# Kernel tuning notes

Hardware: AMD Instinct MI355X
Metric: run time of the kernel (lower is better)

The kernel has to match this reference:

```python
import jax, jax.numpy as jnp
import numpy as np

N = 1024          # n_nodes
F = 32            # n_input_features (per-node embedding dim)
HID = 64          # n_hidden_features
OUT = 32          # n_output_features


def setup_inputs() -> dict:
    key = jax.random.key(0)
    k = jax.random.split(key, 7)
    Edges = jax.random.uniform(k[0], (N, N), dtype=jnp.float32)
    Coordinates = jax.random.normal(k[1], (N, 3), dtype=jnp.float32)
    Embeddings = jax.random.normal(k[2], (N, F), dtype=jnp.float32)
    # nn.Linear params: W (out, in), b (out,)
    s1 = 1.0 / np.sqrt(2 * F)
    s2 = 1.0 / np.sqrt(HID)
    W1 = jax.random.uniform(k[3], (HID, 2 * F), dtype=jnp.float32, minval=-s1, maxval=s1)
    b1 = jax.random.uniform(k[4], (HID,), dtype=jnp.float32, minval=-s1, maxval=s1)
    W2 = jax.random.uniform(k[5], (OUT, HID), dtype=jnp.float32, minval=-s2, maxval=s2)
    b2 = jax.random.uniform(k[6], (OUT,), dtype=jnp.float32, minval=-s2, maxval=s2)
    return {"Edges": Edges, "Coordinates": Coordinates, "Embeddings": Embeddings,
            "W1": W1, "b1": b1, "W2": W2, "b2": b2}


def _swish(x):
    return x * jax.nn.sigmoid(x)


def reference(Edges, Coordinates, Embeddings, W1, b1, W2, b2):
    # pairwise euclidean distances (torch.cdist p=2), grad-safe on the zero diagonal
    diff = Coordinates[:, None, :] - Coordinates[None, :, :]          # (N, N, 3)
    sq = jnp.sum(diff * diff, axis=-1)                                # (N, N)
    dist = jnp.where(sq > 0, jnp.sqrt(jnp.where(sq > 0, sq, 1.0)), 0.0)
    w = Edges * dist                                                  # (N, N)

    # H[i, j] = concat(Emb[i], Emb[j]); first Linear applied without
    # materializing the (N, N, 2F) tensor:
    # (w * [h_i, h_j]) @ W1^T = w * (h_i @ W1[:, :F]^T + h_j @ W1[:, F:]^T)
    A = Embeddings @ W1[:, :F].T                                      # (N, HID) from h_i half
    B = Embeddings @ W1[:, F:].T                                      # (N, HID) from h_j half
    pre1 = w[:, :, None] * (A[:, None, :] + B[None, :, :]) + b1       # (N, N, HID)
    h1 = _swish(pre1)
    pre2 = jnp.einsum('ijh,oh->ijo', h1, W2) + b2                     # (N, N, OUT)
    return _swish(pre2)                                               # squeeze() is a no-op (OUT > 1)
```

## Files before the change

kernel.cpp:

```cpp
#include <hip/hip_runtime.h>
#include <math.h>

#define NN   1024
#define FF   32
#define HID  64
#define OUTF 32

typedef unsigned int  uint;
typedef unsigned short ushort;
typedef __attribute__((ext_vector_type(8)))  __bf16 bf16x8;
typedef __attribute__((ext_vector_type(16))) float  floatx16;

#define WS_A    0
#define WS_B    (WS_A + NN*HID)
#define WS_C4   (WS_B + NN*HID)
#define WS_B1   (WS_C4 + NN*4)
#define WS_B2   (WS_B1 + HID)
#define WS_W2H  (WS_B2 + 64)
#define WS_W2L  (WS_W2H + 1024)

union FragU { ushort u[8]; bf16x8 v; };

__device__ __forceinline__ float swish(float x) {
    float e = __builtin_amdgcn_exp2f(x * -1.442695040888963f);
    return x * __builtin_amdgcn_rcpf(1.0f + e);
}

__global__ void prep_kernel(
    const float* __restrict__ Coords,
    const float* __restrict__ Emb,
    const float* __restrict__ W1,
    const float* __restrict__ b1,
    const float* __restrict__ W2,
    const float* __restrict__ b2,
    float* __restrict__ ws)
{
    const int b = blockIdx.x;
    const int t = threadIdx.x;
    if (b < NN) {
        float accA = 0.f, accB = 0.f;
        const float* w1row = W1 + t * (2 * FF);
        const float* erow  = Emb + b * FF;
        #pragma unroll
        for (int f = 0; f < FF; ++f) {
            float e = erow[f];
            accA = fmaf(e, w1row[f],      accA);
            accB = fmaf(e, w1row[FF + f], accB);
        }
        ws[WS_A + b * HID + t] = accA;
        ws[WS_B + b * HID + t] = accB;
    } else {
        if (t < HID)  ws[WS_B1 + t] = b1[t];
        if (t < OUTF) ws[WS_B2 + t] = b2[t];
        #pragma unroll 1
        for (int n = t; n < NN; n += 64) {
            ws[WS_C4 + n * 4 + 0] = Coords[n * 3 + 0];
            ws[WS_C4 + n * 4 + 1] = Coords[n * 3 + 1];
            ws[WS_C4 + n * 4 + 2] = Coords[n * 3 + 2];
            ws[WS_C4 + n * 4 + 3] = 0.f;
        }
        ushort* w2h = (ushort*)(ws + WS_W2H);
        ushort* w2l = (ushort*)(ws + WS_W2L);
        const int n  = t & 31;
        const int kh = (t >> 5) * 8;
        #pragma unroll
        for (int c = 0; c < 4; ++c) {
            #pragma unroll
            for (int j = 0; j < 8; ++j) {
                const int k = c * 16 + kh + j;
                const float v = W2[n * HID + k];
                const uint  x = __float_as_uint(v);
                const float lo = v - __uint_as_float(x & 0xffff0000u);
                w2h[(c * 64 + t) * 8 + j] = (ushort)(x >> 16);
                w2l[(c * 64 + t) * 8 + j] = (ushort)(__float_as_uint(lo) >> 16);
            }
        }
    }
}

__global__ __launch_bounds__(256) void main_kernel(
    const float* __restrict__ Edges,
    const float* __restrict__ ws,
    float* __restrict__ out)
{
    const int lane = threadIdx.x & 63;
    const int wave = threadIdx.x >> 6;
    const int i    = blockIdx.y;
    const int j0   = blockIdx.x * 128 + wave * 32;
    const int p    = lane & 31;
    const int half = lane >> 5;
    const int jp   = j0 + p;

    const float4 ci = *(const float4*)(ws + WS_C4 + i * 4);
    const float4 cj = *(const float4*)(ws + WS_C4 + jp * 4);
    const float dx = ci.x - cj.x, dy = ci.y - cj.y, dz = ci.z - cj.z;
    const float dist = sqrtf(dx * dx + dy * dy + dz * dz);
    const float w = Edges[i * NN + jp] * dist;

    const ushort* w2hp = (const ushort*)(ws + WS_W2H);
    const ushort* w2lp = (const ushort*)(ws + WS_W2L);
    bf16x8 bh[4], bl[4];
    #pragma unroll
    for (int c = 0; c < 4; ++c) {
        bh[c] = *(const bf16x8*)(w2hp + (c * 64 + lane) * 8);
        bl[c] = *(const bf16x8*)(w2lp + (c * 64 + lane) * 8);
    }

    const float* __restrict__ Ai  = ws + WS_A + i * HID;
    const float* __restrict__ Bj  = ws + WS_B + jp * HID;
    const float* __restrict__ b1f = ws + WS_B1;
    FragU ah[4], al[4];
    #pragma unroll
    for (int c = 0; c < 4; ++c) {
        const int h0 = c * 16 + half * 8;
        float av[8], bv[8], cv[8];
        *(float4*)(av + 0) = *(const float4*)(Ai + h0);
        *(float4*)(av + 4) = *(const float4*)(Ai + h0 + 4);
        *(float4*)(bv + 0) = *(const float4*)(Bj + h0);
        *(float4*)(bv + 4) = *(const float4*)(Bj + h0 + 4);
        *(float4*)(cv + 0) = *(const float4*)(b1f + h0);
        *(float4*)(cv + 4) = *(const float4*)(b1f + h0 + 4);
        #pragma unroll
        for (int j = 0; j < 8; ++j) {
            const float pre = fmaf(w, av[j] + bv[j], cv[j]);
            const float h1  = swish(pre);
            const uint  x   = __float_as_uint(h1);
            const float lo  = h1 - __uint_as_float(x & 0xffff0000u);
            ah[c].u[j] = (ushort)(x >> 16);
            al[c].u[j] = (ushort)(__float_as_uint(lo) >> 16);
        }
    }

    floatx16 acc = {0.f,0.f,0.f,0.f,0.f,0.f,0.f,0.f,0.f,0.f,0.f,0.f,0.f,0.f,0.f,0.f};
    #pragma unroll
    for (int c = 0; c < 4; ++c) {
        acc = __builtin_amdgcn_mfma_f32_32x32x16_bf16(ah[c].v, bh[c], acc, 0, 0, 0);
        acc = __builtin_amdgcn_mfma_f32_32x32x16_bf16(al[c].v, bh[c], acc, 0, 0, 0);
        acc = __builtin_amdgcn_mfma_f32_32x32x16_bf16(ah[c].v, bl[c], acc, 0, 0, 0);
    }

    const float b2n = ws[WS_B2 + p];
    float* __restrict__ ob = out + ((size_t)i * NN + j0) * OUTF + p;
    #pragma unroll
    for (int r = 0; r < 16; ++r) {
        const int m = (r & 3) + 8 * (r >> 2) + 4 * half;
        ob[m * OUTF] = swish(acc[r] + b2n);
    }
}

extern "C" void kernel_launch(void* const* d_in, const int* in_sizes, int n_in,
                              void* d_out, int out_size, void* d_ws, size_t ws_size,
                              hipStream_t stream)
{
    const float* Edges  = (const float*)d_in[0];
    const float* Coords = (const float*)d_in[1];
    const float* Emb    = (const float*)d_in[2];
    const float* W1     = (const float*)d_in[3];
    const float* b1     = (const float*)d_in[4];
    const float* W2     = (const float*)d_in[5];
    const float* b2     = (const float*)d_in[6];
    float* ws  = (float*)d_ws;
    float* out = (float*)d_out;

    hipLaunchKernelGGL(prep_kernel, dim3(NN + 1), dim3(64), 0, stream,
                       Coords, Emb, W1, b1, W2, b2, ws);
    hipLaunchKernelGGL(main_kernel, dim3(NN / 128, NN), dim3(256), 0, stream,
                       Edges, ws, out);
}
```

Measured before the change: 200.7 us.

## Process multiple rows per block to reuse W2, B, and bias registers; nontemporal stores

Each block now loops over four consecutive i rows, so the W2 hi/lo fragments, the per-column B values, b1, b2 and the j coordinates are loaded once and reused across iterations. The grid shrinks by that factor in y. Output stores become nontemporal to avoid polluting cache with the large write-only output. The per-row A loads are now scalar selects by half, which may add instructions, and fewer blocks reduce parallelism slack.

```diff
diff --git a/kernel.cpp b/kernel.cpp
--- a/kernel.cpp
+++ b/kernel.cpp
@@ -5,6 +5,7 @@
 #define FF   32
 #define HID  64
 #define OUTF 32
+#define ITER 4
 
 typedef unsigned int  uint;
 typedef unsigned short ushort;
@@ -85,17 +86,11 @@
 {
     const int lane = threadIdx.x & 63;
     const int wave = threadIdx.x >> 6;
-    const int i    = blockIdx.y;
     const int j0   = blockIdx.x * 128 + wave * 32;
+    const int i0   = blockIdx.y * ITER;
     const int p    = lane & 31;
     const int half = lane >> 5;
     const int jp   = j0 + p;
-
-    const float4 ci = *(const float4*)(ws + WS_C4 + i * 4);
-    const float4 cj = *(const float4*)(ws + WS_C4 + jp * 4);
-    const float dx = ci.x - cj.x, dy = ci.y - cj.y, dz = ci.z - cj.z;
-    const float dist = sqrtf(dx * dx + dy * dy + dz * dz);
-    const float w = Edges[i * NN + jp] * dist;
 
     const ushort* w2hp = (const ushort*)(ws + WS_W2H);
     const ushort* w2lp = (const ushort*)(ws + WS_W2L);
@@ -105,46 +100,65 @@
         bh[c] = *(const bf16x8*)(w2hp + (c * 64 + lane) * 8);
         bl[c] = *(const bf16x8*)(w2lp + (c * 64 + lane) * 8);
     }
-
-    const float* __restrict__ Ai  = ws + WS_A + i * HID;
     const float* __restrict__ Bj  = ws + WS_B + jp * HID;
     const float* __restrict__ b1f = ws + WS_B1;
-    FragU ah[4], al[4];
+    float bv[4][8], b1v[4][8];
     #pragma unroll
     for (int c = 0; c < 4; ++c) {
         const int h0 = c * 16 + half * 8;
-        float av[8], bv[8], cv[8];
-        *(float4*)(av + 0) = *(const float4*)(Ai + h0);
-        *(float4*)(av + 4) = *(const float4*)(Ai + h0 + 4);
-        *(float4*)(bv + 0) = *(const float4*)(Bj + h0);
-        *(float4*)(bv + 4) = *(const float4*)(Bj + h0 + 4);
-        *(float4*)(cv + 0) = *(const float4*)(b1f + h0);
-        *(float4*)(cv + 4) = *(const float4*)(b1f + h0 + 4);
+        *(float4*)(&bv[c][0])  = *(const float4*)(Bj + h0);
+        *(float4*)(&bv[c][4])  = *(const float4*)(Bj + h0 + 4);
+        *(float4*)(&b1v[c][0]) = *(const float4*)(b1f + h0);
+        *(float4*)(&b1v[c][4]) = *(const float4*)(b1f + h0 + 4);
+    }
+    const float4 cj  = *(const float4*)(ws + WS_C4 + jp * 4);
+    const float  b2n = ws[WS_B2 + p];
+
+    #pragma unroll 1
+    for (int it = 0; it < ITER; ++it) {
+        const int i = i0 + it;
+
+        const float cix = ws[WS_C4 + i * 4 + 0];
+        const float ciy = ws[WS_C4 + i * 4 + 1];
+        const float ciz = ws[WS_C4 + i * 4 + 2];
+        const float dx = cix - cj.x, dy = ciy - cj.y, dz = ciz - cj.z;
+        const float dist = sqrtf(dx * dx + dy * dy + dz * dz);
+        const float w = Edges[(size_t)i * NN + jp] * dist;
+
+        const float* __restrict__ Ai = ws + WS_A + (size_t)i * HID;
+
+        FragU ah[4], al[4];
         #pragma unroll
-        for (int j = 0; j < 8; ++j) {
-            const float pre = fmaf(w, av[j] + bv[j], cv[j]);
-            const float h1  = swish(pre);
-            const uint  x   = __float_as_uint(h1);
-            const float lo  = h1 - __uint_as_float(x & 0xffff0000u);
-            ah[c].u[j] = (ushort)(x >> 16);
-            al[c].u[j] = (ushort)(__float_as_uint(lo) >> 16);
+        for (int c = 0; c < 4; ++c) {
+            #pragma unroll
+            for (int jj = 0; jj < 8; ++jj) {
+                const float s_lo = Ai[c * 16 + jj];
+                const float s_hi = Ai[c * 16 + 8 + jj];
+                const float av   = half ? s_hi : s_lo;
+                const float pre  = fmaf(w, av + bv[c][jj], b1v[c][jj]);
+                const float h1   = swish(pre);
+                const uint  x    = __float_as_uint(h1);
+                const float lo   = h1 - __uint_as_float(x & 0xffff0000u);
+                ah[c].u[jj] = (ushort)(x >> 16);
+                al[c].u[jj] = (ushort)(__float_as_uint(lo) >> 16);
+            }
         }
-    }
 
-    floatx16 acc = {0.f,0.f,0.f,0.f,0.f,0.f,0.f,0.f,0.f,0.f,0.f,0.f,0.f,0.f,0.f,0.f};
-    #pragma unroll
-    for (int c = 0; c < 4; ++c) {
-        acc = __builtin_amdgcn_mfma_f32_32x32x16_bf16(ah[c].v, bh[c], acc, 0, 0, 0);
-        acc = __builtin_amdgcn_mfma_f32_32x32x16_bf16(al[c].v, bh[c], acc, 0, 0, 0);
-        acc = __builtin_amdgcn_mfma_f32_32x32x16_bf16(ah[c].v, bl[c], acc, 0, 0, 0);
-    }
+        floatx16 acc = {0.f,0.f,0.f,0.f,0.f,0.f,0.f,0.f,
+                        0.f,0.f,0.f,0.f,0.f,0.f,0.f,0.f};
+        #pragma unroll
+        for (int c = 0; c < 4; ++c) {
+            acc = __builtin_amdgcn_mfma_f32_32x32x16_bf16(ah[c].v, bh[c], acc, 0, 0, 0);
+            acc = __builtin_amdgcn_mfma_f32_32x32x16_bf16(al[c].v, bh[c], acc, 0, 0, 0);
+            acc = __builtin_amdgcn_mfma_f32_32x32x16_bf16(ah[c].v, bl[c], acc, 0, 0, 0);
+        }
 
-    const float b2n = ws[WS_B2 + p];
-    float* __restrict__ ob = out + ((size_t)i * NN + j0) * OUTF + p;
-    #pragma unroll
-    for (int r = 0; r < 16; ++r) {
-        const int m = (r & 3) + 8 * (r >> 2) + 4 * half;
-        ob[m * OUTF] = swish(acc[r] + b2n);
+        float* __restrict__ ob = out + ((size_t)i * NN + j0) * OUTF + p;
+        #pragma unroll
+        for (int r = 0; r < 16; ++r) {
+            const int m = (r & 3) + 8 * (r >> 2) + 4 * half;
+            __builtin_nontemporal_store(swish(acc[r] + b2n), ob + m * OUTF);
+        }
     }
 }
 
@@ -164,6 +178,6 @@
 
     hipLaunchKernelGGL(prep_kernel, dim3(NN + 1), dim3(64), 0, stream,
                        Coords, Emb, W1, b1, W2, b2, ws);
-    hipLaunchKernelGGL(main_kernel, dim3(NN / 128, NN), dim3(256), 0, stream,
+    hipLaunchKernelGGL(main_kernel, dim3(NN / 128, NN / ITER), dim3(256), 0, stream,
                        Edges, ws, out);
 }
```

Measured after the change: 193.6 us. 3.5% less time.
